# Optimization experiments

Measured on AMD Instinct MI355X. Metric: run time of the kernel, lower is better.

The kernel has to match this reference:

```python
import jax, jax.numpy as jnp
import numpy as np

B, S_IMG, S_TXT = 1, 3072, 512
D_MODEL, H, D_HEAD = 3072, 24, 128
INNER = H * D_HEAD
EPS = 1e-5


def rms_norm(x, w):
    # x: [..., D_HEAD]
    var = jnp.mean(jnp.square(x), axis=-1, keepdims=True)
    return x * jax.lax.rsqrt(var + EPS) * w


def apply_rope(x, cos, sin):
    # x: [B,S,H,D]; cos/sin: [S,D]; interleaved (non-neox) rotation
    x1 = x[..., 0::2]
    x2 = x[..., 1::2]
    rot = jnp.stack([-x2, x1], axis=-1).reshape(x.shape)
    c = cos[None, :, None, :]
    s = sin[None, :, None, :]
    return x * c + rot * s


def setup_inputs() -> dict:
    key = jax.random.key(0)
    ks = jax.random.split(key, 12)
    sc = 1.0 / np.sqrt(D_MODEL)
    ang = jax.random.uniform(ks[10], (S_TXT + S_IMG, D_HEAD), jnp.float32, 0.0, 2 * np.pi)
    return {
        "hidden_states": jax.random.normal(ks[0], (B, S_IMG, D_MODEL), jnp.float32),
        "encoder_hidden_states": jax.random.normal(ks[1], (B, S_TXT, D_MODEL), jnp.float32),
        "cos": jnp.cos(ang),
        "sin": jnp.sin(ang),
        "W_qkv": jax.random.normal(ks[2], (3 * INNER, D_MODEL), jnp.float32) * sc,
        "W_add_qkv": jax.random.normal(ks[3], (3 * INNER, D_MODEL), jnp.float32) * sc,
        "b_add_qkv": jnp.zeros((3 * INNER,), jnp.float32),
        "norm_q_w": jnp.ones((D_HEAD,), jnp.float32),
        "norm_k_w": jnp.ones((D_HEAD,), jnp.float32),
        "norm_add_q_w": jnp.ones((D_HEAD,), jnp.float32),
        "norm_add_k_w": jnp.ones((D_HEAD,), jnp.float32),
        "W_out": jax.random.normal(ks[4], (D_MODEL, INNER), jnp.float32) * sc,
        "b_out": jnp.zeros((D_MODEL,), jnp.float32),
        "W_add_out": jax.random.normal(ks[5], (D_MODEL, INNER), jnp.float32) * sc,
        "b_add_out": jnp.zeros((D_MODEL,), jnp.float32),
    }


def reference(hidden_states, encoder_hidden_states, cos, sin,
              W_qkv, W_add_qkv, b_add_qkv,
              norm_q_w, norm_k_w, norm_add_q_w, norm_add_k_w,
              W_out, b_out, W_add_out, b_add_out):
    # fused QKV projections
    qkv = jnp.einsum('bsd,ed->bse', hidden_states, W_qkv)
    q, k, v = jnp.split(qkv, 3, axis=-1)
    eqkv = jnp.einsum('bsd,ed->bse', encoder_hidden_states, W_add_qkv) + b_add_qkv
    eq, ek, ev = jnp.split(eqkv, 3, axis=-1)

    def heads(x):
        return x.reshape(x.shape[0], x.shape[1], H, D_HEAD)

    q, k, v = heads(q), heads(k), heads(v)
    eq, ek, ev = heads(eq), heads(ek), heads(ev)

    # per-head RMSNorm on queries/keys
    q = rms_norm(q, norm_q_w)
    k = rms_norm(k, norm_k_w)
    eq = rms_norm(eq, norm_add_q_w)
    ek = rms_norm(ek, norm_add_k_w)

    # joint concat: text first, then image
    q = jnp.concatenate([eq, q], axis=1)
    k = jnp.concatenate([ek, k], axis=1)
    v = jnp.concatenate([ev, v], axis=1)

    # RoPE on full joint sequence
    q = apply_rope(q, cos, sin)
    k = apply_rope(k, cos, sin)

    # non-causal softmax attention, scale = 1/sqrt(head_dim)
    scale = 1.0 / np.sqrt(D_HEAD)
    scores = jnp.einsum('bqhd,bkhd->bhqk', q, k) * scale
    probs = jax.nn.softmax(scores, axis=-1)
    out = jnp.einsum('bhqk,bkhd->bqhd', probs, v)  # [B,S,H,D]
    out = out.reshape(out.shape[0], out.shape[1], INNER)

    enc_out = out[:, :S_TXT]
    img_out = out[:, S_TXT:]
    enc_out = jnp.einsum('bse,de->bsd', enc_out, W_add_out) + b_add_out
    img_out = jnp.einsum('bse,de->bsd', img_out, W_out) + b_out
    return (img_out, enc_out)
```

## Files before the change

kernel.cpp:

```cpp
#include <hip/hip_runtime.h>


typedef unsigned short u16;
typedef __attribute__((ext_vector_type(2))) unsigned short u16x2;
typedef __attribute__((ext_vector_type(4))) unsigned short u16x4;
typedef __attribute__((ext_vector_type(8))) unsigned short u16x8;
typedef __attribute__((ext_vector_type(8))) short bf16x8;
typedef __attribute__((ext_vector_type(4))) float f32x4;
typedef __attribute__((ext_vector_type(16))) float f32x16;
typedef __attribute__((ext_vector_type(4))) unsigned u32x4;

#define DEV __device__ __forceinline__

DEV u16 f2bf(float f) {
  unsigned u = __builtin_bit_cast(unsigned, f);
  u = (u + 0x7FFFu + ((u >> 16) & 1u)) >> 16;
  return (u16)u;
}
DEV float bf2f(u16 s) { return __builtin_bit_cast(float, (unsigned)s << 16); }

DEV void store_out(u16* p, float v)  { *p = f2bf(v); }
DEV void store_out(float* p, float v) { *p = v; }

#define AS1(p) (const __attribute__((address_space(1))) void*)(p)
#define AS3(p) (__attribute__((address_space(3))) void*)(p)
#define GLL16(g, l) __builtin_amdgcn_global_load_lds(AS1(g), AS3(l), 16, 0, 0)

#define BAR() do { asm volatile("" ::: "memory"); __builtin_amdgcn_s_barrier(); \
                   asm volatile("" ::: "memory"); } while (0)
#define VMC8() asm volatile("s_waitcnt vmcnt(8)" ::: "memory")
#define VMC0() asm volatile("s_waitcnt vmcnt(0)" ::: "memory")

__global__ __launch_bounds__(256) void cvt_kernel(const float* __restrict__ src,
                                                  u16* __restrict__ dst, int n4) {
  int i = blockIdx.x * blockDim.x + threadIdx.x;
  int stride = gridDim.x * blockDim.x;
  for (; i < n4; i += stride) {
    float4 v = reinterpret_cast<const float4*>(src)[i];
    u16x4 o;
    o.x = f2bf(v.x); o.y = f2bf(v.y); o.z = f2bf(v.z); o.w = f2bf(v.w);
    reinterpret_cast<u16x4*>(dst)[i] = o;
  }
}

template <typename OT>
__global__ __launch_bounds__(512, 2) void gemm256(
    const u16* __restrict__ A,
    const u16* __restrict__ Bimg, const u16* __restrict__ Benc,
    const float* __restrict__ biasImg, const float* __restrict__ biasEnc,
    OT* __restrict__ Cimg, OT* __restrict__ Cenc,
    int N, int K, int split, int nwg) {
  const int bid = blockIdx.x;
  const int swz = (bid & 7) * (nwg >> 3) + (bid >> 3);
  const int ntn = N >> 8;
  const int mt = swz / ntn, nt = swz % ntn;
  const int m0 = mt << 8, n0 = nt << 8;
  const u16* B = (m0 < split) ? Benc : Bimg;
  const float* bias = (m0 < split) ? biasEnc : biasImg;

  __shared__ u16 lds[2][2][16384];

  const int tid = threadIdx.x, w = tid >> 6, lane = tid & 63;
  const int wm = w >> 2, wn = w & 3;
  const int q = lane & 15, hi = lane >> 4;
  const size_t ldb = (size_t)K * 2;

  f32x4 acc[8][4];
#pragma unroll
  for (int i = 0; i < 8; ++i)
#pragma unroll
    for (int j = 0; j < 4; ++j)
#pragma unroll
      for (int r = 0; r < 4; ++r) acc[i][j][r] = 0.f;

  auto STAGE = [&](int d, int kt) {
    const char* sA = (const char*)A + (size_t)m0 * ldb + kt * 128;
    const char* sB = (const char*)B + (size_t)n0 * ldb + kt * 128;
    char* dA = (char*)&lds[d][0][0];
    char* dB = (char*)&lds[d][1][0];
#pragma unroll
    for (int j = 0; j < 4; ++j) {
      int base = j * 8192 + w * 1024;
      int off = base + lane * 16;
      int row = off >> 7;
      int src = (off & 127) ^ ((row & 7) << 4);
      GLL16(sA + (size_t)row * ldb + src, dA + base);
      GLL16(sB + (size_t)row * ldb + src, dB + base);
    }
  };
  auto LDA = [&](int d, int i, int ks) -> bf16x8 {
    int row = wm * 128 + i * 16 + q;
    int cb = ks * 64 + hi * 16;
    return *(const bf16x8*)((const char*)&lds[d][0][0] + row * 128 + (cb ^ ((row & 7) << 4)));
  };
  auto LDB = [&](int d, int j, int ks) -> bf16x8 {
    int row = wn * 64 + j * 16 + q;
    int cb = ks * 64 + hi * 16;
    return *(const bf16x8*)((const char*)&lds[d][1][0] + row * 128 + (cb ^ ((row & 7) << 4)));
  };

  auto HALF = [&](int d) {
    bf16x8 bfr[4][2];
#pragma unroll
    for (int ph = 0; ph < 4; ++ph) {
      if (ph == 0) {
#pragma unroll
        for (int j = 0; j < 4; ++j)
#pragma unroll
          for (int ks = 0; ks < 2; ++ks) bfr[j][ks] = LDB(d, j, ks);
      }
      bf16x8 af[2][2];
#pragma unroll
      for (int m = 0; m < 2; ++m)
#pragma unroll
        for (int ks = 0; ks < 2; ++ks) af[m][ks] = LDA(d, 2 * ph + m, ks);
      __builtin_amdgcn_s_setprio(1);
#pragma unroll
      for (int m = 0; m < 2; ++m)
#pragma unroll
        for (int j = 0; j < 4; ++j)
#pragma unroll
          for (int ks = 0; ks < 2; ++ks)
            acc[2 * ph + m][j] = __builtin_amdgcn_mfma_f32_16x16x32_bf16(
                af[m][ks], bfr[j][ks], acc[2 * ph + m][j], 0, 0, 0);
      __builtin_amdgcn_s_setprio(0);
      if (ph < 3) BAR();
    }
  };

  const int NT2 = K >> 7;
  STAGE(0, 0);
  STAGE(1, 1);
  VMC8();
  BAR();
  for (int t = 0; t < NT2; ++t) {
    HALF(0);
    BAR();
    if (t + 1 < NT2) { STAGE(0, 2 * t + 2); VMC8(); }
    else             VMC0();
    BAR();
    HALF(1);
    BAR();
    if (t + 1 < NT2) { STAGE(1, 2 * t + 3); VMC8(); }
    else             VMC0();
    BAR();
  }

#pragma unroll
  for (int i = 0; i < 8; ++i) {
    int rbase = m0 + wm * 128 + i * 16 + (hi << 2);
#pragma unroll
    for (int j = 0; j < 4; ++j) {
      int col = n0 + wn * 64 + j * 16 + q;
      float bv = bias ? bias[col] : 0.f;
#pragma unroll
      for (int r = 0; r < 4; ++r) {
        int row = rbase + r;
        float v = acc[i][j][r] + bv;
        if (row < split) store_out(&Cenc[(size_t)row * N + col], v);
        else             store_out(&Cimg[(size_t)(row - split) * N + col], v);
      }
    }
  }
}

__global__ __launch_bounds__(256) void norm_rope(
    u16* __restrict__ qkv, u16* __restrict__ vt,
    const float* __restrict__ cosT, const float* __restrict__ sinT,
    const float* __restrict__ nqw_img, const float* __restrict__ nkw_img,
    const float* __restrict__ nqw_enc, const float* __restrict__ nkw_enc) {
  const int h = blockIdx.y;
  const int s0 = blockIdx.x * 64;
  const int tid = threadIdx.x, w = tid >> 6, lane = tid & 63;
  const bool enc = (s0 < 512);
  const float* nqw = enc ? nqw_enc : nqw_img;
  const float* nkw = enc ? nkw_enc : nkw_img;
  const float SCL = 0.12751743f;
  const float wq0 = nqw[2 * lane], wq1 = nqw[2 * lane + 1];
  const float wk0 = nkw[2 * lane], wk1 = nkw[2 * lane + 1];
  u16x8 va0, va1, vb0, vb1;
#pragma unroll
  for (int r = 0; r < 16; ++r) {
    const int s = s0 + w * 16 + r;
    const size_t rowb = (size_t)s * 9216 + h * 128 + 2 * lane;
    float2 cv = *(const float2*)&cosT[(size_t)s * 128 + 2 * lane];
    float2 sv = *(const float2*)&sinT[(size_t)s * 128 + 2 * lane];
    {
      u16x2 qu = *(u16x2*)&qkv[rowb];
      float x0 = bf2f(qu.x), x1 = bf2f(qu.y);
      float ss = x0 * x0 + x1 * x1;
#pragma unroll
      for (int d = 1; d < 64; d <<= 1) ss += __shfl_xor(ss, d);
      float rms = rsqrtf(ss * (1.0f / 128.0f) + 1e-5f);
      x0 *= rms * wq0; x1 *= rms * wq1;
      float o0 = (x0 * cv.x - x1 * sv.x) * SCL;
      float o1 = (x1 * cv.y + x0 * sv.y) * SCL;
      u16x2 ou; ou.x = f2bf(o0); ou.y = f2bf(o1);
      *(u16x2*)&qkv[rowb] = ou;
    }
    {
      u16x2 ku = *(u16x2*)&qkv[rowb + 3072];
      float x0 = bf2f(ku.x), x1 = bf2f(ku.y);
      float ss = x0 * x0 + x1 * x1;
#pragma unroll
      for (int d = 1; d < 64; d <<= 1) ss += __shfl_xor(ss, d);
      float rms = rsqrtf(ss * (1.0f / 128.0f) + 1e-5f);
      x0 *= rms * wk0; x1 *= rms * wk1;
      float o0 = x0 * cv.x - x1 * sv.x;
      float o1 = x1 * cv.y + x0 * sv.y;
      u16x2 ou; ou.x = f2bf(o0); ou.y = f2bf(o1);
      *(u16x2*)&qkv[rowb + 3072] = ou;
    }
    {
      u16x2 vu = *(u16x2*)&qkv[rowb + 6144];
      if (r < 8) { va0[r] = vu.x; vb0[r] = vu.y; }
      else       { va1[r - 8] = vu.x; vb1[r - 8] = vu.y; }
    }
  }
  const size_t vbase = (size_t)h * 128 * 3584 + (size_t)(2 * lane) * 3584 + s0 + w * 16;
  *(u16x8*)&vt[vbase]            = va0;
  *(u16x8*)&vt[vbase + 8]        = va1;
  *(u16x8*)&vt[vbase + 3584]     = vb0;
  *(u16x8*)&vt[vbase + 3584 + 8] = vb1;
}

__global__ __launch_bounds__(256, 2) void attn_kernel(
    const u16* __restrict__ qkv, const u16* __restrict__ vt,
    u16* __restrict__ aout) {
  const int bid = blockIdx.x;
  const int qt = bid / 24;
  const int rr = bid % 24;
  const int h = (rr % 8) * 3 + (rr / 8);
  const int tid = threadIdx.x, w = tid >> 6, lane = tid & 63;
  const int q32 = lane & 31, hi5 = lane >> 5;
  const int qbase = qt * 128 + w * 32;
  __shared__ u16 Klds[2][8192];
  __shared__ u16 Vlds[2][8192];

  bf16x8 aq[8];
  {
    const u16* qp = qkv + (size_t)(qbase + q32) * 9216 + h * 128 + hi5 * 8;
#pragma unroll
    for (int ds = 0; ds < 8; ++ds) aq[ds] = *(const bf16x8*)(qp + ds * 16);
  }
  float m_i = -1e30f, l_i = 0.f;
  f32x16 o[4];
#pragma unroll
  for (int dt = 0; dt < 4; ++dt)
#pragma unroll
    for (int r = 0; r < 16; ++r) o[dt][r] = 0.f;
  const size_t vhead = (size_t)h * 128 * 3584;

  auto STAGE_K = [&](int kt0, int b) {
    const int kt = w >> 1;
    const char* src = (const char*)(qkv + (size_t)(kt0 + kt * 32 + q32) * 9216 + 3072 + h * 128) + hi5 * 16;
    char* dst = (char*)Klds[b] + kt * 8192 + (w & 1) * 4096 + lane * 16;
#pragma unroll
    for (int j = 0; j < 4; ++j)
      GLL16(src + ((w & 1) * 4 + j) * 32, dst + j * 1024);
  };
  auto STAGE_V = [&](int kt0, int b) {
    const char* src = (const char*)(vt + vhead + (size_t)(w * 32 + q32) * 3584 + kt0) + hi5 * 16;
    char* dst = (char*)Vlds[b] + w * 4096 + lane * 16;
#pragma unroll
    for (int j = 0; j < 4; ++j)
      GLL16(src + j * 32, dst + j * 1024);
  };

  auto PACK = [&](const float* p, bf16x8* out2) {
    unsigned w0[4], w1[4];
#pragma unroll
    for (int g = 0; g < 4; ++g) {
      asm("v_cvt_pk_bf16_f32 %0, %1, %2" : "=v"(w0[g]) : "v"(p[4 * g + 0]), "v"(p[4 * g + 1]));
      asm("v_cvt_pk_bf16_f32 %0, %1, %2" : "=v"(w1[g]) : "v"(p[4 * g + 2]), "v"(p[4 * g + 3]));
    }
    asm("v_permlane32_swap_b32 %0, %1" : "+v"(w0[0]), "+v"(w0[1]));
    asm("v_permlane32_swap_b32 %0, %1" : "+v"(w1[0]), "+v"(w1[1]));
    asm("v_permlane32_swap_b32 %0, %1" : "+v"(w0[2]), "+v"(w0[3]));
    asm("v_permlane32_swap_b32 %0, %1" : "+v"(w1[2]), "+v"(w1[3]));
    u32x4 lo = {w0[0], w1[0], w0[1], w1[1]};
    u32x4 hi_ = {w0[2], w1[2], w0[3], w1[3]};
    out2[0] = __builtin_bit_cast(bf16x8, lo);
    out2[1] = __builtin_bit_cast(bf16x8, hi_);
  };

  const int NT = 56;
  STAGE_K(0, 0);   STAGE_V(0, 0);
  STAGE_K(64, 1);  STAGE_V(64, 1);
  for (int t = 0; t < NT; ++t) {
    const int b = t & 1;
    if (t + 1 < NT) VMC8(); else VMC0();
    BAR();

    f32x16 s0, s1;
#pragma unroll
    for (int r = 0; r < 16; ++r) { s0[r] = 0.f; s1[r] = 0.f; }
    __builtin_amdgcn_s_setprio(1);
#pragma unroll
    for (int ds = 0; ds < 8; ++ds) {
      bf16x8 k0 = *(const bf16x8*)((const char*)Klds[b] + ds * 1024 + lane * 16);
      bf16x8 k1 = *(const bf16x8*)((const char*)Klds[b] + 8192 + ds * 1024 + lane * 16);
      s0 = __builtin_amdgcn_mfma_f32_32x32x16_bf16(k0, aq[ds], s0, 0, 0, 0);
      s1 = __builtin_amdgcn_mfma_f32_32x32x16_bf16(k1, aq[ds], s1, 0, 0, 0);
    }
    __builtin_amdgcn_s_setprio(0);

    float mx = s0[0];
#pragma unroll
    for (int r = 1; r < 16; ++r) mx = fmaxf(mx, s0[r]);
#pragma unroll
    for (int r = 0; r < 16; ++r) mx = fmaxf(mx, s1[r]);
    mx = fmaxf(mx, __shfl_xor(mx, 32));
    if (!__all(mx - m_i <= 8.f)) {
      float mnew = fmaxf(m_i, mx);
      float alpha = __builtin_amdgcn_exp2f(m_i - mnew);
      m_i = mnew;
      l_i *= alpha;
#pragma unroll
      for (int r = 0; r < 16; ++r) {
        int qr = (r & 3) + 8 * (r >> 2) + 4 * hi5;
        float ar = __shfl(alpha, qr);
#pragma unroll
        for (int dt = 0; dt < 4; ++dt) o[dt][r] *= ar;
      }
    }
    float p0[16], p1[16];
    float psum = 0.f;
#pragma unroll
    for (int r = 0; r < 16; ++r) { p0[r] = __builtin_amdgcn_exp2f(s0[r] - m_i); psum += p0[r]; }
#pragma unroll
    for (int r = 0; r < 16; ++r) { p1[r] = __builtin_amdgcn_exp2f(s1[r] - m_i); psum += p1[r]; }
    psum += __shfl_xor(psum, 32);
    l_i += psum;

    bf16x8 pa[4];
    PACK(p0, &pa[0]);
    PACK(p1, &pa[2]);

    __builtin_amdgcn_s_setprio(1);
#pragma unroll
    for (int dt = 0; dt < 4; ++dt) {
#pragma unroll
      for (int ks = 0; ks < 4; ++ks) {
        bf16x8 bv = *(const bf16x8*)((const char*)Vlds[b] + dt * 4096 + ks * 1024 + lane * 16);
        o[dt] = __builtin_amdgcn_mfma_f32_32x32x16_bf16(pa[ks], bv, o[dt], 0, 0, 0);
      }
    }
    __builtin_amdgcn_s_setprio(0);
    BAR();
    if (t + 2 < NT) { STAGE_K((t + 2) * 64, b); STAGE_V((t + 2) * 64, b); }
  }

#pragma unroll
  for (int r = 0; r < 16; ++r) {
    const int qr = (r & 3) + 8 * (r >> 2) + 4 * hi5;
    const float lr = __shfl(l_i, qr);
    const float inv = 1.0f / lr;
    const size_t srow = (size_t)(qbase + qr) * 3072 + h * 128 + q32;
#pragma unroll
    for (int dt = 0; dt < 4; ++dt)
      aout[srow + dt * 32] = f2bf(o[dt][r] * inv);
  }
}

extern "C" void kernel_launch(void* const* d_in, const int* in_sizes, int n_in,
                              void* d_out, int out_size, void* d_ws, size_t ws_size,
                              hipStream_t stream) {
  (void)in_sizes; (void)n_in; (void)out_size; (void)ws_size;
  const float* hs    = (const float*)d_in[0];
  const float* ehs   = (const float*)d_in[1];
  const float* cosT  = (const float*)d_in[2];
  const float* sinT  = (const float*)d_in[3];
  const float* Wqkv  = (const float*)d_in[4];
  const float* Wadd  = (const float*)d_in[5];
  const float* bAdd  = (const float*)d_in[6];
  const float* nqw   = (const float*)d_in[7];
  const float* nkw   = (const float*)d_in[8];
  const float* naqw  = (const float*)d_in[9];
  const float* nakw  = (const float*)d_in[10];
  const float* Wout  = (const float*)d_in[11];
  const float* bout  = (const float*)d_in[12];
  const float* Waddo = (const float*)d_in[13];
  const float* baddo = (const float*)d_in[14];

  char* ws = (char*)d_ws;
  u16* Ain = (u16*)(ws);
  u16* WqI = (u16*)(ws + 22020096);
  u16* WqE = WqI + (size_t)9216 * 3072;
  u16* WoI = (u16*)(ws + 135266304);
  u16* WoE = WoI + (size_t)3072 * 3072;
  u16* qkv = (u16*)(ws + 173015040);
  u16* vt   = Ain;
  u16* aout = WqI;

  cvt_kernel<<<1024, 256, 0, stream>>>(ehs,   Ain,                      512 * 3072 / 4);
  cvt_kernel<<<1024, 256, 0, stream>>>(hs,    Ain + (size_t)512 * 3072, 3072 * 3072 / 4);
  cvt_kernel<<<2048, 256, 0, stream>>>(Wqkv,  WqI, 9216 * 3072 / 4);
  cvt_kernel<<<2048, 256, 0, stream>>>(Wadd,  WqE, 9216 * 3072 / 4);
  cvt_kernel<<<1024, 256, 0, stream>>>(Wout,  WoI, 3072 * 3072 / 4);
  cvt_kernel<<<1024, 256, 0, stream>>>(Waddo, WoE, 3072 * 3072 / 4);

  gemm256<u16><<<dim3(504), 512, 0, stream>>>(Ain, WqI, WqE, nullptr, bAdd,
                                              qkv + (size_t)512 * 9216, qkv, 9216, 3072, 512, 504);
  norm_rope<<<dim3(56, 24), 256, 0, stream>>>(qkv, vt, cosT, sinT, nqw, nkw, naqw, nakw);
  attn_kernel<<<dim3(672), 256, 0, stream>>>(qkv, vt, aout);
  float* outp = (float*)d_out;
  gemm256<float><<<dim3(168), 512, 0, stream>>>(aout, WoI, WoE, bout, baddo,
                                                outp, outp + (size_t)3072 * 3072, 3072, 3072, 512, 168);
}
```

Measured before the change: 705.7 us.

## Halve attention KV tile to 32 keys and raise occupancy to 4 blocks

The attention kernel now processes 32 keys per iteration instead of 64. This halves the K/V LDS double buffers, drops the second score accumulator, and raises the launch bound to 4 blocks per CU. Staging loads, the waitcnt depth and the V layout indexing are reworked to match the smaller tile. The aim is higher occupancy and lower register/LDS pressure to hide latency, at the cost of twice as many iterations, barriers and softmax rescale checks.

Measured after the change: 814.6 us. +15.4%, slower.

```diff
diff --git a/kernel.cpp b/kernel.cpp
--- a/kernel.cpp
+++ b/kernel.cpp
@@ -29,6 +29,7 @@
 #define BAR() do { asm volatile("" ::: "memory"); __builtin_amdgcn_s_barrier(); \
                    asm volatile("" ::: "memory"); } while (0)
 #define VMC8() asm volatile("s_waitcnt vmcnt(8)" ::: "memory")
+#define VMC4() asm volatile("s_waitcnt vmcnt(4)" ::: "memory")
 #define VMC0() asm volatile("s_waitcnt vmcnt(0)" ::: "memory")
 
 __global__ __launch_bounds__(256) void cvt_kernel(const float* __restrict__ src,
@@ -224,7 +225,7 @@
   *(u16x8*)&vt[vbase + 3584 + 8] = vb1;
 }
 
-__global__ __launch_bounds__(256, 2) void attn_kernel(
+__global__ __launch_bounds__(256, 4) void attn_kernel(
     const u16* __restrict__ qkv, const u16* __restrict__ vt,
     u16* __restrict__ aout) {
   const int bid = blockIdx.x;
@@ -234,8 +235,8 @@
   const int tid = threadIdx.x, w = tid >> 6, lane = tid & 63;
   const int q32 = lane & 31, hi5 = lane >> 5;
   const int qbase = qt * 128 + w * 32;
-  __shared__ u16 Klds[2][8192];
-  __shared__ u16 Vlds[2][8192];
+  __shared__ u16 Klds[2][4096];
+  __shared__ u16 Vlds[2][4096];
 
   bf16x8 aq[8];
   {
@@ -252,19 +253,20 @@
   const size_t vhead = (size_t)h * 128 * 3584;
 
   auto STAGE_K = [&](int kt0, int b) {
-    const int kt = w >> 1;
-    const char* src = (const char*)(qkv + (size_t)(kt0 + kt * 32 + q32) * 9216 + 3072 + h * 128) + hi5 * 16;
-    char* dst = (char*)Klds[b] + kt * 8192 + (w & 1) * 4096 + lane * 16;
-#pragma unroll
-    for (int j = 0; j < 4; ++j)
-      GLL16(src + ((w & 1) * 4 + j) * 32, dst + j * 1024);
+    const char* src = (const char*)(qkv + (size_t)(kt0 + q32) * 9216 + 3072 + h * 128) + hi5 * 16;
+    char* dst = (char*)Klds[b] + w * 2048 + lane * 16;
+#pragma unroll
+    for (int j = 0; j < 2; ++j)
+      GLL16(src + (w * 2 + j) * 32, dst + j * 1024);
   };
   auto STAGE_V = [&](int kt0, int b) {
-    const char* src = (const char*)(vt + vhead + (size_t)(w * 32 + q32) * 3584 + kt0) + hi5 * 16;
-    char* dst = (char*)Vlds[b] + w * 4096 + lane * 16;
-#pragma unroll
-    for (int j = 0; j < 4; ++j)
-      GLL16(src + j * 32, dst + j * 1024);
+    char* dst = (char*)Vlds[b] + w * 2048 + lane * 16;
+#pragma unroll
+    for (int j = 0; j < 2; ++j) {
+      const int u = w * 2 + j, dt = u >> 1, ks = u & 1;
+      GLL16((const char*)(vt + vhead + (size_t)(dt * 32 + q32) * 3584 + kt0) + ks * 32 + hi5 * 16,
+            dst + j * 1024);
+    }
   };
 
   auto PACK = [&](const float* p, bf16x8* out2) {
@@ -284,32 +286,28 @@
     out2[1] = __builtin_bit_cast(bf16x8, hi_);
   };
 
-  const int NT = 56;
+  const int NT = 112;
   STAGE_K(0, 0);   STAGE_V(0, 0);
-  STAGE_K(64, 1);  STAGE_V(64, 1);
+  STAGE_K(32, 1);  STAGE_V(32, 1);
   for (int t = 0; t < NT; ++t) {
     const int b = t & 1;
-    if (t + 1 < NT) VMC8(); else VMC0();
-    BAR();
-
-    f32x16 s0, s1;
-#pragma unroll
-    for (int r = 0; r < 16; ++r) { s0[r] = 0.f; s1[r] = 0.f; }
+    if (t + 1 < NT) VMC4(); else VMC0();
+    BAR();
+
+    f32x16 s0;
+#pragma unroll
+    for (int r = 0; r < 16; ++r) s0[r] = 0.f;
     __builtin_amdgcn_s_setprio(1);
 #pragma unroll
     for (int ds = 0; ds < 8; ++ds) {
       bf16x8 k0 = *(const bf16x8*)((const char*)Klds[b] + ds * 1024 + lane * 16);
-      bf16x8 k1 = *(const bf16x8*)((const char*)Klds[b] + 8192 + ds * 1024 + lane * 16);
       s0 = __builtin_amdgcn_mfma_f32_32x32x16_bf16(k0, aq[ds], s0, 0, 0, 0);
-      s1 = __builtin_amdgcn_mfma_f32_32x32x16_bf16(k1, aq[ds], s1, 0, 0, 0);
     }
     __builtin_amdgcn_s_setprio(0);
 
     float mx = s0[0];
 #pragma unroll
     for (int r = 1; r < 16; ++r) mx = fmaxf(mx, s0[r]);
-#pragma unroll
-    for (int r = 0; r < 16; ++r) mx = fmaxf(mx, s1[r]);
     mx = fmaxf(mx, __shfl_xor(mx, 32));
     if (!__all(mx - m_i <= 8.f)) {
       float mnew = fmaxf(m_i, mx);
@@ -324,31 +322,28 @@
         for (int dt = 0; dt < 4; ++dt) o[dt][r] *= ar;
       }
     }
-    float p0[16], p1[16];
+    float p0[16];
     float psum = 0.f;
 #pragma unroll
     for (int r = 0; r < 16; ++r) { p0[r] = __builtin_amdgcn_exp2f(s0[r] - m_i); psum += p0[r]; }
-#pragma unroll
-    for (int r = 0; r < 16; ++r) { p1[r] = __builtin_amdgcn_exp2f(s1[r] - m_i); psum += p1[r]; }
     psum += __shfl_xor(psum, 32);
     l_i += psum;
 
-    bf16x8 pa[4];
-    PACK(p0, &pa[0]);
-    PACK(p1, &pa[2]);
+    bf16x8 pa[2];
+    PACK(p0, pa);
 
     __builtin_amdgcn_s_setprio(1);
 #pragma unroll
     for (int dt = 0; dt < 4; ++dt) {
 #pragma unroll
-      for (int ks = 0; ks < 4; ++ks) {
-        bf16x8 bv = *(const bf16x8*)((const char*)Vlds[b] + dt * 4096 + ks * 1024 + lane * 16);
+      for (int ks = 0; ks < 2; ++ks) {
+        bf16x8 bv = *(const bf16x8*)((const char*)Vlds[b] + (dt * 2 + ks) * 1024 + lane * 16);
         o[dt] = __builtin_amdgcn_mfma_f32_32x32x16_bf16(pa[ks], bv, o[dt], 0, 0, 0);
       }
     }
     __builtin_amdgcn_s_setprio(0);
     BAR();
-    if (t + 2 < NT) { STAGE_K((t + 2) * 64, b); STAGE_V((t + 2) * 64, b); }
+    if (t + 2 < NT) { STAGE_K((t + 2) * 32, b); STAGE_V((t + 2) * 32, b); }
   }
 
 #pragma unroll
```
